# Performance work log

Measured on AMD Instinct MI355X. Metric: run time of the kernel, lower is better.

The kernel has to match this reference:

```python
import jax, jax.numpy as jnp
import numpy as np

N_QUBITS = 12
N_LAYERS = 6
BATCH = 2048
N_OUTPUTS = 2
C64 = jnp.complex64


def setup_inputs() -> dict:
    key = jax.random.key(0)
    k1, k2 = jax.random.split(key)
    x = jax.random.normal(k1, (BATCH, N_QUBITS), dtype=jnp.float32)
    # nn.Parameter: torch.randn(n_layers, n_qubits, 3) * 0.1
    weights = jax.random.normal(k2, (N_LAYERS, N_QUBITS, 3), dtype=jnp.float32) * 0.1
    return {"x": x, "weights": weights}


def _rx(t):
    # t: (...,) angles -> (..., 2, 2) RX matrices
    c = jnp.cos(t * 0.5).astype(C64)
    s = (-1j * jnp.sin(t * 0.5)).astype(C64)
    return jnp.stack([jnp.stack([c, s], -1), jnp.stack([s, c], -1)], -2)


def _ry(t):
    c = jnp.cos(t * 0.5).astype(C64)
    s = jnp.sin(t * 0.5).astype(C64)
    return jnp.stack([jnp.stack([c, -s], -1), jnp.stack([s, c], -1)], -2)


def _rz(t):
    e = jnp.exp(-0.5j * t).astype(C64)
    z = jnp.zeros_like(e)
    return jnp.stack([jnp.stack([e, z], -1), jnp.stack([z, jnp.conj(e)], -1)], -2)


def _rot(w):
    # PennyLane Rot(phi, theta, omega) = RZ(omega) @ RY(theta) @ RZ(phi); w: (n_qubits, 3)
    return _rz(w[:, 2]) @ _ry(w[:, 1]) @ _rz(w[:, 0])


def _apply_1q(state, gate, q):
    # state: (B, 2**n) complex; gate: (2,2) or (B,2,2); qubit q (wire 0 = MSB)
    B = state.shape[0]
    s = state.reshape(B, 2 ** q, 2, -1)
    if gate.ndim == 3:
        s = jnp.einsum('bij,bljr->blir', gate, s)
    else:
        s = jnp.einsum('ij,bljr->blir', gate, s)
    return s.reshape(B, -1)


def _apply_cnot(state, c, t, n):
    # control c, target t; flip target axis where control bit == 1
    B = state.shape[0]
    s = state.reshape((B,) + (2,) * n)
    ac, at = 1 + c, 1 + t
    s0 = jnp.take(s, 0, axis=ac)
    s1 = jnp.take(s, 1, axis=ac)
    at2 = at - 1 if at > ac else at
    s1 = jnp.flip(s1, axis=at2)
    s = jnp.stack([s0, s1], axis=ac)
    return s.reshape(B, -1)


def _layer(state, w, n):
    # strongly-entangling layer: Rot on every wire, then full CNOT entanglement
    rot = _rot(w)  # (n, 2, 2)
    for q in range(n):
        state = _apply_1q(state, rot[q], q)
    for i in range(n):
        for j in range(i + 1, n):
            state = _apply_cnot(state, i, j, n)
    return state


def _forward(x, weights):
    n = N_QUBITS
    B = x.shape[0]
    state = jnp.zeros((B, 2 ** n), C64).at[:, 0].set(1.0)
    # angle encoding: RX(x_q) on wire q (PennyLane AngleEmbedding default axis X)
    for q in range(n):
        state = _apply_1q(state, _rx(x[:, q]), q)
    layer_ckpt = jax.checkpoint(lambda s, w: _layer(s, w, n))
    for l in range(N_LAYERS):
        state = layer_ckpt(state, weights[l])
    # expval(PauliZ) on wires 0..n_outputs-1
    probs = state.real ** 2 + state.imag ** 2  # (B, 2**n)
    outs = []
    for k in range(N_OUTPUTS):
        p = probs.reshape(B, 2 ** k, 2, -1)
        outs.append(p[:, :, 0, :].sum((1, 2)) - p[:, :, 1, :].sum((1, 2)))
    return jnp.stack(outs, -1)  # (B, n_outputs)


def reference(x, weights):
    return _forward(x, weights)
```

## Files before the change

kernel.cpp:

```cpp
#include <hip/hip_runtime.h>
#include <math.h>

#define NQ 12
#define DIM 4096
#define NL 6
#define TPB 256


#define WS_WA0 0
#define WS_W   512
#define WS_ZA0 3072
#define WS_ZM  3104
#define WS_RYT 3424
#define WS_FLOATS 3712

typedef float f2 __attribute__((ext_vector_type(2)));

__device__ __forceinline__ f2 pk_mul(f2 a, f2 b) {
  f2 d; asm("v_pk_mul_f32 %0, %1, %2" : "=v"(d) : "v"(a), "v"(b)); return d;
}
__device__ __forceinline__ f2 pk_fma(f2 a, f2 b, f2 c) {
  f2 d; asm("v_pk_fma_f32 %0, %1, %2, %3" : "=v"(d) : "v"(a), "v"(b), "v"(c)); return d;
}
__device__ __forceinline__ f2 cmulp(f2 a, f2 c) {
  f2 r1, d;
  asm("v_pk_mul_f32 %0, %1, %2 op_sel:[0,0] op_sel_hi:[0,1]"
      : "=v"(r1) : "v"(a), "v"(c));
  asm("v_pk_fma_f32 %0, %1, %2, %3 op_sel:[1,1,0] op_sel_hi:[1,0,1] neg_lo:[1,0,0]"
      : "=v"(d) : "v"(a), "v"(c), "v"(r1));
  return d;
}

template<int BIT>
__device__ __forceinline__ void apply_ry16(f2 v[16], f2 cc, f2 ss) {
  #pragma unroll
  for (int j = 0; j < 16; ++j) {
    if (j & (1 << BIT)) continue;
    const int k = j | (1 << BIT);
    f2 a = v[j], b = v[k];
    f2 t1 = pk_mul(a, cc);
    f2 t2 = pk_mul(a, ss);
    f2 na; asm("v_pk_fma_f32 %0, %1, %2, %3 neg_lo:[1,0,0] neg_hi:[1,0,0]"
               : "=v"(na) : "v"(b), "v"(ss), "v"(t1));
    f2 nb = pk_fma(b, cc, t2);
    v[j] = na; v[k] = nb;
  }
}

__global__ __launch_bounds__(256)
void qprep_kernel(const float* __restrict__ w, float* __restrict__ ws) {
  const int t = threadIdx.x;

  {
    float f = 0.f;
    #pragma unroll
    for (int k = 0; k < 8; ++k) {
      float p = w[(0*NQ + 7 - k)*3 + 0];
      f += ((t >> k) & 1) ? 0.5f*p : -0.5f*p;
    }
    float sv, cv; sincosf(f, &sv, &cv);
    ws[WS_WA0 + 2*t] = cv; ws[WS_WA0 + 2*t + 1] = sv;
  }

  #pragma unroll 1
  for (int l = 0; l < NL-1; ++l) {
    float f = 0.f;
    const int gt = t ^ (t >> 1);
    #pragma unroll
    for (int k = 0; k < 8; ++k) {
      float om = w[(l*NQ + 11 - k)*3 + 2];
      f += ((t >> k) & 1) ? 0.5f*om : -0.5f*om;
    }
    #pragma unroll
    for (int k = 0; k < 7; ++k) {
      float ph = w[((l+1)*NQ + 11 - k)*3 + 0];
      f += ((gt >> k) & 1) ? 0.5f*ph : -0.5f*ph;
    }
    float sv, cv; sincosf(f, &sv, &cv);
    ws[WS_W + (l*256 + t)*2] = cv; ws[WS_W + (l*256 + t)*2 + 1] = sv;
  }

  if (t < 16) {
    float f = 0.f;
    #pragma unroll
    for (int m = 0; m < 4; ++m) {
      float p = w[(0*NQ + 11 - m)*3 + 0];
      f += ((t >> m) & 1) ? 0.5f*p : -0.5f*p;
    }
    float sv, cv; sincosf(f, &sv, &cv);
    ws[WS_ZA0 + 2*t] = cv; ws[WS_ZA0 + 2*t + 1] = sv;
  }

  if (t < 160) {
    const int l = t >> 5, h = (t >> 4) & 1, j = t & 15;
    float f = 0.f;
    #pragma unroll
    for (int m = 0; m < 4; ++m) {
      float om = w[(l*NQ + 3 - m)*3 + 2];
      f += ((j >> m) & 1) ? 0.5f*om : -0.5f*om;
    }
    {
      float p4 = w[((l+1)*NQ + 4)*3 + 0];
      f += (h ^ (j & 1)) ? 0.5f*p4 : -0.5f*p4;
    }
    const int gj = j ^ (j >> 1);
    #pragma unroll
    for (int m = 0; m < 4; ++m) {
      float ph = w[((l+1)*NQ + 3 - m)*3 + 0];
      f += ((gj >> m) & 1) ? 0.5f*ph : -0.5f*ph;
    }
    float sv, cv; sincosf(f, &sv, &cv);
    ws[WS_ZM + 2*t] = cv; ws[WS_ZM + 2*t + 1] = sv;
  }

  if (t < 72) {
    float sv, cv; sincosf(0.5f*w[t*3 + 1], &sv, &cv);
    ((float4*)(ws + WS_RYT))[t] = make_float4(cv, cv, sv, sv);
  }
}

__global__ __launch_bounds__(TPB, 5)
void qsim12_kernel(const float* __restrict__ x, const float* __restrict__ ws,
                   float* __restrict__ out) {
  __shared__ __align__(16) float st[2*DIM];

  const int t = threadIdx.x;
  const int b = blockIdx.x;
  char* stb = (char*)st;

  float csx[NQ], csy[NQ];
  {
    const int q = t & 63;
    float xv = (q < NQ) ? x[b*NQ + q] : 0.f;
    float sv, cv; sincosf(0.5f*xv, &sv, &cv);
    #pragma unroll
    for (int qq = 0; qq < NQ; ++qq) {
      csx[qq] = __int_as_float(__builtin_amdgcn_readlane(__float_as_int(cv), qq));
      csy[qq] = __int_as_float(__builtin_amdgcn_readlane(__float_as_int(sv), qq));
    }
  }

  int baseA[8], baseB[8];
  #pragma unroll
  for (int m = 0; m < 8; ++m) {
    baseA[m] = (t << 7) + (((2*m) ^ (t & 14)) << 3);
    baseB[m] = ((t >> 4) << 11) + ((((t & 15) ^ (2*m))) << 3);
  }
  const int baseC = ((t >> 4) << 7) + ((((t & 15) ^ ((t >> 4) & 15))) << 3);
  const int G = t ^ (t >> 1);
  int baseS[2];
  #pragma unroll
  for (int par = 0; par < 2; ++par) {
    const int k8 = par << 3;
    baseS[par] = ((((G >> 4) & 15) ^ k8) << 7)
               + ((((G & 15) ^ ((G >> 4) & 14) ^ k8)) << 3);
  }

  f2 v[16];

  {
    float rhi = 1.f;
    #pragma unroll
    for (int k = 0; k < 8; ++k)
      rhi *= ((t >> k) & 1) ? csy[7-k] : csx[7-k];
    const int popt = __popc(t);
    #pragma unroll
    for (int j = 0; j < 16; ++j) {
      float r = rhi;
      #pragma unroll
      for (int m = 0; m < 4; ++m)
        r *= ((j >> m) & 1) ? csy[11-m] : csx[11-m];
      const int pj = (popt + __popc(j)) & 3;
      if      (pj == 0) v[j] = (f2){ r, 0.f};
      else if (pj == 1) v[j] = (f2){0.f, -r};
      else if (pj == 2) v[j] = (f2){-r, 0.f};
      else              v[j] = (f2){0.f,  r};
    }
  }

  #define RY(BIT, WQ)                                                     \
    { const float4 r = *(const float4*)(ws + WS_RYT + 4*(l*NQ + (WQ)));   \
      apply_ry16<BIT>(v, (f2){r.x, r.y}, (f2){r.z, r.w}); }

  #pragma unroll 1
  for (int l = 0; l < NL; ++l) {
    if (l > 0) {
      #pragma unroll
      for (int m = 0; m < 8; ++m) {
        float4 q4 = *(const float4*)(stb + baseA[m]);
        v[2*m]   = (f2){q4.x, q4.y};
        v[2*m+1] = (f2){q4.z, q4.w};
      }
    } else {
      const float2 wv = *(const float2*)(ws + WS_WA0 + 2*t);
      const f2 wA0 = (f2){wv.x, wv.y};
      #pragma unroll
      for (int j = 0; j < 16; ++j) {
        const float2 zv = *(const float2*)(ws + WS_ZA0 + 2*j);
        v[j] = cmulp(cmulp(v[j], (f2){zv.x, zv.y}), wA0);
      }
    }
    RY(0,11) RY(1,10) RY(2,9) RY(3,8)
    #pragma unroll
    for (int m = 0; m < 8; ++m)
      *(float4*)(stb + baseA[m]) =
          make_float4(v[2*m].x, v[2*m].y, v[2*m+1].x, v[2*m+1].y);
    __syncthreads();

    #pragma unroll
    for (int m = 0; m < 8; ++m) {
      v[2*m]   = *(const f2*)(stb + baseB[m] + (2*m)*128);
      v[2*m+1] = *(const f2*)(stb + baseB[m] + (2*m+1)*128);
    }
    RY(0,7) RY(1,6) RY(2,5) RY(3,4)
    #pragma unroll
    for (int m = 0; m < 8; ++m) {
      *(f2*)(stb + baseB[m] + (2*m)*128)         = v[2*m];
      *(f2*)(stb + (baseB[m] ^ 8) + (2*m+1)*128) = v[2*m+1];
    }
    __syncthreads();

    #pragma unroll
    for (int j = 0; j < 16; ++j)
      v[j] = *(const f2*)(stb + baseC + j*2048);
    RY(0,3) RY(1,2) RY(2,1) RY(3,0)
    if (l < NL-1) {
      const float2 wv = *(const float2*)(ws + WS_W + (l*TPB + t)*2);
      const f2 W = (f2){wv.x, wv.y};
      const float* zmb = ws + WS_ZM + ((l*2 + ((t >> 7) & 1))*16)*2;
      #pragma unroll
      for (int j = 0; j < 16; ++j) {
        const float2 zv = *(const float2*)(zmb + 2*j);
        v[j] = cmulp(cmulp(v[j], (f2){zv.x, zv.y}), W);
      }
      #pragma unroll
      for (int j = 0; j < 16; ++j) {
        const int g4 = (j ^ (j >> 1)) & 15;
        *(f2*)(stb + baseS[j & 1] + (g4 << 11)) = v[j];
      }
      __syncthreads();
    }
  }

  float a0 = 0.f, a1 = 0.f;
  #pragma unroll
  for (int j = 0; j < 16; ++j) {
    float pr = v[j].x*v[j].x + v[j].y*v[j].y;
    a0 += ((j >> 3) & 1) ? -pr : pr;
    a1 += (((j >> 2) ^ (j >> 3)) & 1) ? -pr : pr;
  }
  #pragma unroll
  for (int off = 32; off >= 1; off >>= 1) {
    a0 += __shfl_down(a0, off);
    a1 += __shfl_down(a1, off);
  }
  __syncthreads();
  if ((t & 63) == 0) { st[(t >> 6)*2] = a0; st[(t >> 6)*2 + 1] = a1; }
  __syncthreads();
  if (t == 0) {
    out[b*2 + 0] = st[0] + st[2] + st[4] + st[6];
    out[b*2 + 1] = st[1] + st[3] + st[5] + st[7];
  }
}

extern "C" void kernel_launch(void* const* d_in, const int* in_sizes, int n_in,
                              void* d_out, int out_size, void* d_ws, size_t ws_size,
                              hipStream_t stream) {
  const float* x = (const float*)d_in[0];
  const float* w = (const float*)d_in[1];
  float* out = (float*)d_out;
  float* ws = (float*)d_ws;
  int B = in_sizes[0] / NQ;
  qprep_kernel<<<1, 256, 0, stream>>>(w, ws);
  qsim12_kernel<<<B, TPB, 0, stream>>>(x, ws, out);
}
```

Baseline: 128.9 us.

## Simulate each sample with one 64-thread wave holding 64 amplitudes per lane

Reshapes the per-sample state vector simulation from 256 threads with 16 amplitudes each and three shared-memory transposes per layer into a single 64-lane wave holding 64 amplitudes per lane, with two 6-qubit RY passes and one transpose per layer. The diagonal RZ/CNOT phase tables are recomputed on a 6+6 qubit split, and the final reduction becomes a single wave shuffle with no block barrier. This removes cross-wave barriers and some LDS traffic, but needs 128+ VGPRs for the state, lowers waves per block, and keeps 32KB of LDS per wave, which limits occupancy.

```diff
diff --git a/kernel.cpp b/kernel.cpp
--- a/kernel.cpp
+++ b/kernel.cpp
@@ -4,15 +4,14 @@
 #define NQ 12
 #define DIM 4096
 #define NL 6
-#define TPB 256
+#define TPB 64
 
 
 #define WS_WA0 0
-#define WS_W   512
-#define WS_ZA0 3072
-#define WS_ZM  3104
-#define WS_RYT 3424
-#define WS_FLOATS 3712
+#define WS_Z0  128
+#define WS_W   256
+#define WS_Z   896
+#define WS_RYT 2176
 
 typedef float f2 __attribute__((ext_vector_type(2)));
 
@@ -32,9 +31,9 @@
 }
 
 template<int BIT>
-__device__ __forceinline__ void apply_ry16(f2 v[16], f2 cc, f2 ss) {
+__device__ __forceinline__ void apply_ry64(f2 v[64], f2 cc, f2 ss) {
   #pragma unroll
-  for (int j = 0; j < 16; ++j) {
+  for (int j = 0; j < 64; ++j) {
     if (j & (1 << BIT)) continue;
     const int k = j | (1 << BIT);
     f2 a = v[j], b = v[k];
@@ -50,217 +49,194 @@
 __global__ __launch_bounds__(256)
 void qprep_kernel(const float* __restrict__ w, float* __restrict__ ws) {
   const int t = threadIdx.x;
-
-  {
-    float f = 0.f;
-    #pragma unroll
-    for (int k = 0; k < 8; ++k) {
-      float p = w[(0*NQ + 7 - k)*3 + 0];
-      f += ((t >> k) & 1) ? 0.5f*p : -0.5f*p;
-    }
-    float sv, cv; sincosf(f, &sv, &cv);
-    ws[WS_WA0 + 2*t] = cv; ws[WS_WA0 + 2*t + 1] = sv;
-  }
-
-  #pragma unroll 1
-  for (int l = 0; l < NL-1; ++l) {
-    float f = 0.f;
-    const int gt = t ^ (t >> 1);
-    #pragma unroll
-    for (int k = 0; k < 8; ++k) {
-      float om = w[(l*NQ + 11 - k)*3 + 2];
-      f += ((t >> k) & 1) ? 0.5f*om : -0.5f*om;
-    }
-    #pragma unroll
-    for (int k = 0; k < 7; ++k) {
-      float ph = w[((l+1)*NQ + 11 - k)*3 + 0];
-      f += ((gt >> k) & 1) ? 0.5f*ph : -0.5f*ph;
-    }
-    float sv, cv; sincosf(f, &sv, &cv);
-    ws[WS_W + (l*256 + t)*2] = cv; ws[WS_W + (l*256 + t)*2 + 1] = sv;
-  }
-
-  if (t < 16) {
-    float f = 0.f;
-    #pragma unroll
-    for (int m = 0; m < 4; ++m) {
-      float p = w[(0*NQ + 11 - m)*3 + 0];
-      f += ((t >> m) & 1) ? 0.5f*p : -0.5f*p;
-    }
-    float sv, cv; sincosf(f, &sv, &cv);
-    ws[WS_ZA0 + 2*t] = cv; ws[WS_ZA0 + 2*t + 1] = sv;
-  }
-
-  if (t < 160) {
-    const int l = t >> 5, h = (t >> 4) & 1, j = t & 15;
-    float f = 0.f;
-    #pragma unroll
-    for (int m = 0; m < 4; ++m) {
-      float om = w[(l*NQ + 3 - m)*3 + 2];
-      f += ((j >> m) & 1) ? 0.5f*om : -0.5f*om;
-    }
-    {
-      float p4 = w[((l+1)*NQ + 4)*3 + 0];
-      f += (h ^ (j & 1)) ? 0.5f*p4 : -0.5f*p4;
-    }
-    const int gj = j ^ (j >> 1);
-    #pragma unroll
-    for (int m = 0; m < 4; ++m) {
-      float ph = w[((l+1)*NQ + 3 - m)*3 + 0];
-      f += ((gj >> m) & 1) ? 0.5f*ph : -0.5f*ph;
-    }
-    float sv, cv; sincosf(f, &sv, &cv);
-    ws[WS_ZM + 2*t] = cv; ws[WS_ZM + 2*t + 1] = sv;
-  }
-
-  if (t < 72) {
+  const float HPI = 1.57079632679489662f;
+
+  if (t < 64) {
+    const int u = t;
+    float f = 0.f;
+    #pragma unroll
+    for (int k = 0; k < 6; ++k) {
+      float p = w[(0*NQ + (11-k))*3 + 0];
+      f += ((u >> k) & 1) ? 0.5f*p : -0.5f*p;
+    }
+    f -= HPI * (float)__popc(u);
+    float sv, cv; sincosf(f, &sv, &cv);
+    ws[WS_WA0 + 2*u] = cv; ws[WS_WA0 + 2*u + 1] = sv;
+  } else if (t < 128) {
+    const int p_ = t - 64;
+    float f = 0.f;
+    #pragma unroll
+    for (int k = 0; k < 6; ++k) {
+      float p = w[(0*NQ + (5-k))*3 + 0];
+      f += ((p_ >> k) & 1) ? 0.5f*p : -0.5f*p;
+    }
+    f -= HPI * (float)__popc(p_);
+    float sv, cv; sincosf(f, &sv, &cv);
+    ws[WS_Z0 + 2*p_] = cv; ws[WS_Z0 + 2*p_ + 1] = sv;
+  }
+
+  for (int idx = t; idx < 5*64; idx += 256) {
+    const int l = idx >> 6, u = idx & 63;
+    float f = 0.f;
+    #pragma unroll
+    for (int k = 0; k < 6; ++k) {
+      float om = w[(l*NQ + (5-k))*3 + 2];
+      f += ((u >> k) & 1) ? 0.5f*om : -0.5f*om;
+    }
+    const int gu = u ^ (u >> 1);
+    #pragma unroll
+    for (int k = 0; k < 6; ++k) {
+      float ph = w[((l+1)*NQ + (5-k))*3 + 0];
+      f += ((gu >> k) & 1) ? 0.5f*ph : -0.5f*ph;
+    }
+    float sv, cv; sincosf(f, &sv, &cv);
+    ws[WS_W + 2*idx] = cv; ws[WS_W + 2*idx + 1] = sv;
+  }
+
+  for (int idx = t; idx < 5*2*64; idx += 256) {
+    const int l = idx >> 7, h = (idx >> 6) & 1, p_ = idx & 63;
+    float f = 0.f;
+    #pragma unroll
+    for (int k = 0; k < 6; ++k) {
+      float om = w[(l*NQ + (11-k))*3 + 2];
+      f += ((p_ >> k) & 1) ? 0.5f*om : -0.5f*om;
+    }
+    const int gp = (p_ ^ (p_ >> 1)) ^ (h << 5);
+    #pragma unroll
+    for (int k = 0; k < 6; ++k) {
+      float ph = w[((l+1)*NQ + (11-k))*3 + 0];
+      f += ((gp >> k) & 1) ? 0.5f*ph : -0.5f*ph;
+    }
+    float sv, cv; sincosf(f, &sv, &cv);
+    ws[WS_Z + 2*idx] = cv; ws[WS_Z + 2*idx + 1] = sv;
+  }
+
+  if (t < NL*NQ) {
     float sv, cv; sincosf(0.5f*w[t*3 + 1], &sv, &cv);
     ((float4*)(ws + WS_RYT))[t] = make_float4(cv, cv, sv, sv);
   }
 }
 
-__global__ __launch_bounds__(TPB, 5)
+__global__ __launch_bounds__(TPB, 1)
 void qsim12_kernel(const float* __restrict__ x, const float* __restrict__ ws,
                    float* __restrict__ out) {
   __shared__ __align__(16) float st[2*DIM];
-
-  const int t = threadIdx.x;
+  const int L = threadIdx.x;
   const int b = blockIdx.x;
   char* stb = (char*)st;
 
   float csx[NQ], csy[NQ];
   {
-    const int q = t & 63;
-    float xv = (q < NQ) ? x[b*NQ + q] : 0.f;
+    float xv = (L < NQ) ? x[b*NQ + L] : 0.f;
     float sv, cv; sincosf(0.5f*xv, &sv, &cv);
     #pragma unroll
-    for (int qq = 0; qq < NQ; ++qq) {
-      csx[qq] = __int_as_float(__builtin_amdgcn_readlane(__float_as_int(cv), qq));
-      csy[qq] = __int_as_float(__builtin_amdgcn_readlane(__float_as_int(sv), qq));
-    }
-  }
-
-  int baseA[8], baseB[8];
-  #pragma unroll
-  for (int m = 0; m < 8; ++m) {
-    baseA[m] = (t << 7) + (((2*m) ^ (t & 14)) << 3);
-    baseB[m] = ((t >> 4) << 11) + ((((t & 15) ^ (2*m))) << 3);
-  }
-  const int baseC = ((t >> 4) << 7) + ((((t & 15) ^ ((t >> 4) & 15))) << 3);
-  const int G = t ^ (t >> 1);
-  int baseS[2];
-  #pragma unroll
-  for (int par = 0; par < 2; ++par) {
-    const int k8 = par << 3;
-    baseS[par] = ((((G >> 4) & 15) ^ k8) << 7)
-               + ((((G & 15) ^ ((G >> 4) & 14) ^ k8)) << 3);
-  }
-
-  f2 v[16];
+    for (int q = 0; q < NQ; ++q) {
+      csx[q] = __int_as_float(__builtin_amdgcn_readlane(__float_as_int(cv), q));
+      csy[q] = __int_as_float(__builtin_amdgcn_readlane(__float_as_int(sv), q));
+    }
+  }
+
+  f2 v[64];
 
   {
-    float rhi = 1.f;
-    #pragma unroll
-    for (int k = 0; k < 8; ++k)
-      rhi *= ((t >> k) & 1) ? csy[7-k] : csx[7-k];
-    const int popt = __popc(t);
-    #pragma unroll
-    for (int j = 0; j < 16; ++j) {
-      float r = rhi;
-      #pragma unroll
-      for (int m = 0; m < 4; ++m)
-        r *= ((j >> m) & 1) ? csy[11-m] : csx[11-m];
-      const int pj = (popt + __popc(j)) & 3;
-      if      (pj == 0) v[j] = (f2){ r, 0.f};
-      else if (pj == 1) v[j] = (f2){0.f, -r};
-      else if (pj == 2) v[j] = (f2){-r, 0.f};
-      else              v[j] = (f2){0.f,  r};
-    }
-  }
-
-  #define RY(BIT, WQ)                                                     \
-    { const float4 r = *(const float4*)(ws + WS_RYT + 4*(l*NQ + (WQ)));   \
-      apply_ry16<BIT>(v, (f2){r.x, r.y}, (f2){r.z, r.w}); }
+    float rl = 1.f;
+    #pragma unroll
+    for (int k = 0; k < 6; ++k)
+      rl *= ((L >> k) & 1) ? csy[11-k] : csx[11-k];
+    float mlo[8], mhi[8];
+    #pragma unroll
+    for (int pm = 0; pm < 8; ++pm) {
+      float a = ((pm >> 0) & 1) ? csy[5] : csx[5];
+      a *= ((pm >> 1) & 1) ? csy[4] : csx[4];
+      a *= ((pm >> 2) & 1) ? csy[3] : csx[3];
+      mlo[pm] = a;
+      float bb = ((pm >> 0) & 1) ? csy[2] : csx[2];
+      bb *= ((pm >> 1) & 1) ? csy[1] : csx[1];
+      bb *= ((pm >> 2) & 1) ? csy[0] : csx[0];
+      mhi[pm] = bb;
+    }
+    const float2 wv = *(const float2*)(ws + WS_WA0 + 2*L);
+    const f2 a0 = (f2){wv.x*rl, wv.y*rl};
+    #pragma unroll
+    for (int p = 0; p < 64; ++p) {
+      const float2 zv = *(const float2*)(ws + WS_Z0 + 2*p);
+      f2 ph = cmulp(a0, (f2){zv.x, zv.y});
+      const float m = mlo[p & 7] * mhi[p >> 3];
+      v[p] = pk_mul(ph, (f2){m, m});
+    }
+  }
+
+  #define RY6(BIT, WQ) { const float4 r = *(const float4*)(ws + WS_RYT + 4*(l*NQ + (WQ))); \
+      apply_ry64<BIT>(v, (f2){r.x, r.y}, (f2){r.z, r.w}); }
 
   #pragma unroll 1
   for (int l = 0; l < NL; ++l) {
     if (l > 0) {
       #pragma unroll
-      for (int m = 0; m < 8; ++m) {
-        float4 q4 = *(const float4*)(stb + baseA[m]);
-        v[2*m]   = (f2){q4.x, q4.y};
-        v[2*m+1] = (f2){q4.z, q4.w};
-      }
-    } else {
-      const float2 wv = *(const float2*)(ws + WS_WA0 + 2*t);
-      const f2 wA0 = (f2){wv.x, wv.y};
+      for (int r = 0; r < 64; ++r)
+        v[r] = *(const f2*)(stb + r*512 + ((L ^ (r & 62)) << 3));
+    }
+    RY6(0,5) RY6(1,4) RY6(2,3) RY6(3,2) RY6(4,1) RY6(5,0)
+
+    #pragma unroll
+    for (int m = 0; m < 32; ++m) {
+      const int idx = (2*m) ^ (L & 62);
+      *(float4*)(stb + L*512 + (idx << 3)) =
+          make_float4(v[2*m].x, v[2*m].y, v[2*m+1].x, v[2*m+1].y);
+    }
+    __syncthreads();
+    #pragma unroll
+    for (int p = 0; p < 64; ++p)
+      v[p] = *(const f2*)(stb + p*512 + ((L ^ (p & 62)) << 3));
+
+    RY6(0,11) RY6(1,10) RY6(2,9) RY6(3,8) RY6(4,7) RY6(5,6)
+
+    if (l < NL-1) {
+      const float2 wv = *(const float2*)(ws + WS_W + (l*64 + L)*2);
+      const f2 W = (f2){wv.x, wv.y};
+      const float* zb = ws + WS_Z + ((l*2 + (L & 1))*64)*2;
       #pragma unroll
-      for (int j = 0; j < 16; ++j) {
-        const float2 zv = *(const float2*)(ws + WS_ZA0 + 2*j);
-        v[j] = cmulp(cmulp(v[j], (f2){zv.x, zv.y}), wA0);
-      }
-    }
-    RY(0,11) RY(1,10) RY(2,9) RY(3,8)
-    #pragma unroll
-    for (int m = 0; m < 8; ++m)
-      *(float4*)(stb + baseA[m]) =
-          make_float4(v[2*m].x, v[2*m].y, v[2*m+1].x, v[2*m+1].y);
-    __syncthreads();
-
-    #pragma unroll
-    for (int m = 0; m < 8; ++m) {
-      v[2*m]   = *(const f2*)(stb + baseB[m] + (2*m)*128);
-      v[2*m+1] = *(const f2*)(stb + baseB[m] + (2*m+1)*128);
-    }
-    RY(0,7) RY(1,6) RY(2,5) RY(3,4)
-    #pragma unroll
-    for (int m = 0; m < 8; ++m) {
-      *(f2*)(stb + baseB[m] + (2*m)*128)         = v[2*m];
-      *(f2*)(stb + (baseB[m] ^ 8) + (2*m+1)*128) = v[2*m+1];
-    }
-    __syncthreads();
-
-    #pragma unroll
-    for (int j = 0; j < 16; ++j)
-      v[j] = *(const f2*)(stb + baseC + j*2048);
-    RY(0,3) RY(1,2) RY(2,1) RY(3,0)
-    if (l < NL-1) {
-      const float2 wv = *(const float2*)(ws + WS_W + (l*TPB + t)*2);
-      const f2 W = (f2){wv.x, wv.y};
-      const float* zmb = ws + WS_ZM + ((l*2 + ((t >> 7) & 1))*16)*2;
-      #pragma unroll
-      for (int j = 0; j < 16; ++j) {
-        const float2 zv = *(const float2*)(zmb + 2*j);
-        v[j] = cmulp(cmulp(v[j], (f2){zv.x, zv.y}), W);
-      }
-      #pragma unroll
-      for (int j = 0; j < 16; ++j) {
-        const int g4 = (j ^ (j >> 1)) & 15;
-        *(f2*)(stb + baseS[j & 1] + (g4 << 11)) = v[j];
+      for (int p0 = 0; p0 < 64; p0 += 8) {
+        f2 z[8];
+        #pragma unroll
+        for (int q = 0; q < 8; ++q) {
+          const float2 zv = *(const float2*)(zb + 2*(p0+q));
+          z[q] = (f2){zv.x, zv.y};
+        }
+        #pragma unroll
+        for (int q = 0; q < 8; ++q)
+          v[p0+q] = cmulp(cmulp(v[p0+q], z[q]), W);
       }
       __syncthreads();
-    }
-  }
-
-  float a0 = 0.f, a1 = 0.f;
+
+      const int Gh  = (L ^ (L >> 1)) & 63;
+      const int hb5 = (L & 1) << 5;
+      const int gsw = Gh & 62;
+      #pragma unroll
+      for (int m = 0; m < 32; ++m) {
+        const int glo0 = ((2*m) ^ m) ^ hb5;
+        const int e = glo0 & ~1;
+        float4 q4;
+        if (m & 1) q4 = make_float4(v[2*m+1].x, v[2*m+1].y, v[2*m].x, v[2*m].y);
+        else       q4 = make_float4(v[2*m].x, v[2*m].y, v[2*m+1].x, v[2*m+1].y);
+        *(float4*)(stb + Gh*512 + ((e ^ gsw) << 3)) = q4;
+      }
+      __syncthreads();
+    }
+  }
+
+  float ssum = 0.f;
   #pragma unroll
-  for (int j = 0; j < 16; ++j) {
-    float pr = v[j].x*v[j].x + v[j].y*v[j].y;
-    a0 += ((j >> 3) & 1) ? -pr : pr;
-    a1 += (((j >> 2) ^ (j >> 3)) & 1) ? -pr : pr;
-  }
+  for (int p = 0; p < 64; ++p)
+    ssum += v[p].x*v[p].x + v[p].y*v[p].y;
+  float s0 = ((L >> 5) & 1) ? -ssum : ssum;
+  float s1 = (((L >> 4) ^ (L >> 5)) & 1) ? -ssum : ssum;
   #pragma unroll
   for (int off = 32; off >= 1; off >>= 1) {
-    a0 += __shfl_down(a0, off);
-    a1 += __shfl_down(a1, off);
-  }
-  __syncthreads();
-  if ((t & 63) == 0) { st[(t >> 6)*2] = a0; st[(t >> 6)*2 + 1] = a1; }
-  __syncthreads();
-  if (t == 0) {
-    out[b*2 + 0] = st[0] + st[2] + st[4] + st[6];
-    out[b*2 + 1] = st[1] + st[3] + st[5] + st[7];
-  }
+    s0 += __shfl_down(s0, off);
+    s1 += __shfl_down(s1, off);
+  }
+  if (L == 0) { out[b*2 + 0] = s0; out[b*2 + 1] = s1; }
 }
 
 extern "C" void kernel_launch(void* const* d_in, const int* in_sizes, int n_in,
```

Result: slower. 155.3 us (+20.5%).
